# Kernel optimization log

Hardware: AMD Instinct MI355X
Metric: run time of the kernel (lower is better)

The kernel has to match this reference:

```python
import jax, jax.numpy as jnp
import numpy as np

T, H, I, E, K = 2048, 2048, 1408, 8, 2


def setup_inputs() -> dict:
    key = jax.random.key(0)
    k1, k2, k3, k4, k5 = jax.random.split(key, 5)
    s_h = 1.0 / np.sqrt(H)
    s_i = 1.0 / np.sqrt(I)
    return {
        "hidden_states": jax.random.normal(k1, (T, H), dtype=jnp.float32),
        "router_logits": jax.random.normal(k2, (T, E), dtype=jnp.float32),
        "Wg": jax.random.normal(k3, (E, H, I), dtype=jnp.float32) * s_h,
        "Wu": jax.random.normal(k4, (E, H, I), dtype=jnp.float32) * s_h,
        "Wd": jax.random.normal(k5, (E, I, H), dtype=jnp.float32) * s_i,
        "top_k": K,
    }


def reference(hidden_states, router_logits, Wg, Wu, Wd, top_k):
    # top-k routing: softmax over the selected top-k logits (as in torch.topk + softmax)
    topk_vals, topk_ids = jax.lax.top_k(router_logits, top_k)  # [T,K]
    topk_w = jax.nn.softmax(topk_vals, axis=-1)                # [T,K]

    n_tok = hidden_states.shape[0]
    n_exp = router_logits.shape[-1]
    # combine weights [T,E]: scatter top-k weights back to expert slots
    cw = jnp.zeros((n_tok, n_exp), hidden_states.dtype)
    cw = cw.at[jnp.arange(n_tok)[:, None], topk_ids].add(topk_w)

    out = jnp.zeros_like(hidden_states)
    for e in range(n_exp):  # small fixed expert count
        g = hidden_states @ Wg[e]          # [T,I]
        u = hidden_states @ Wu[e]          # [T,I]
        y = (jax.nn.silu(g) * u) @ Wd[e]   # [T,H]
        out = out + cw[:, e:e + 1] * y
    return out
```

## Files before the change

### kernel.cpp

```cpp
#include <hip/hip_runtime.h>
#include <hip/hip_bf16.h>
#include <cstdint>
#include <cstddef>

#define TT 2048
#define HH 2048
#define II 1408
#define EE 8
#define MAXROWS 5120

typedef unsigned short u16;
typedef __attribute__((ext_vector_type(8))) __bf16 bf16x8;
typedef __attribute__((ext_vector_type(4))) float f32x4;

typedef const __attribute__((address_space(1))) uint32_t* gas1_t;
typedef __attribute__((address_space(3))) uint32_t* las3_t;

__device__ __forceinline__ float bf2f(u16 b) {
    return __uint_as_float(((uint32_t)b) << 16);
}
__device__ __forceinline__ u16 f2bf(float x) {
    uint32_t u = __float_as_uint(x);
    u += 0x7fffu + ((u >> 16) & 1u);
    return (u16)(u >> 16);
}

__global__ void k_sniff(const u16* __restrict__ raw, int* __restrict__ flag) {
    __shared__ int cnt;
    if (threadIdx.x == 0) cnt = 0;
    __syncthreads();
    int w = 0;
    for (int i = threadIdx.x; i < 4096; i += 256) {
        u16 x = raw[i];
        if (x & 0x7fff) {
            int ex = (x >> 7) & 0xff;
            if (ex == 0xff || ex < 100 || ex > 140) ++w;
        }
    }
    atomicAdd(&cnt, w);
    __syncthreads();
    if (threadIdx.x == 0) flag[0] = (cnt > 100) ? 1 : 0;
}

__global__ void k_zero(float* __restrict__ out_acc, int* __restrict__ counts) {
    const int i0 = (blockIdx.x * 256 + threadIdx.x) * 4;
    *(float4*)&out_acc[i0] = make_float4(0.f, 0.f, 0.f, 0.f);
    if (blockIdx.x == 0 && threadIdx.x < EE) counts[threadIdx.x] = 0;
}

__global__ void k_routing2(const void* __restrict__ logits, const int* __restrict__ flag,
                           int* __restrict__ counts, int* __restrict__ idx,
                           float* __restrict__ wt) {
    int t = blockIdx.x * 256 + threadIdx.x;
    if (t >= TT) return;
    const int f = flag[0];
    float v[EE];
#pragma unroll
    for (int e = 0; e < EE; ++e)
        v[e] = f ? ((const float*)logits)[t * EE + e]
                 : bf2f(((const u16*)logits)[t * EE + e]);
    int i0 = 0; float v0 = v[0];
#pragma unroll
    for (int e = 1; e < EE; ++e) { if (v[e] > v0) { v0 = v[e]; i0 = e; } }
    int i1 = -1; float v1 = -3.4e38f;
#pragma unroll
    for (int e = 0; e < EE; ++e) { if (e != i0 && v[e] > v1) { v1 = v[e]; i1 = e; } }
    float r = __expf(v1 - v0);
    float s = 1.f / (1.f + r);
    int p0 = atomicAdd(&counts[i0], 1);
    idx[i0 * TT + p0] = t; wt[i0 * TT + p0] = s;
    int p1 = atomicAdd(&counts[i1], 1);
    idx[i1 * TT + p1] = t; wt[i1 * TT + p1] = r * s;
}

__global__ void k_offsets(const int* __restrict__ counts, int* __restrict__ meta) {
    if (threadIdx.x == 0 && blockIdx.x == 0) {
        int off = 0;
        for (int e = 0; e < EE; ++e) {
            int c = counts[e];
            int p = (c + 127) & ~127;
            meta[e] = off; meta[8 + e] = p;
            off += p;
        }
    }
}

__global__ void k_cast(const void* __restrict__ src, const int* __restrict__ flag,
                       u16* __restrict__ dst) {
    const int i0 = (blockIdx.x * 256 + threadIdx.x) * 8;
    if (flag[0]) {
        const float* s = (const float*)src;
#pragma unroll
        for (int j = 0; j < 8; ++j) dst[i0 + j] = f2bf(s[i0 + j]);
    } else {
        const u16* s = (const u16*)src;
        *(uint4*)&dst[i0] = *(const uint4*)&s[i0];
    }
}

__global__ void k_transposeV(const void* __restrict__ src, const int* __restrict__ flag,
                             u16* __restrict__ dst, int R, int C) {
    __shared__ u16 t[64][68];
    const size_t eo = (size_t)blockIdx.z * (size_t)R * (size_t)C;
    const int r0 = blockIdx.y * 64, c0 = blockIdx.x * 64;
    const int tid = threadIdx.x;
    const int f = flag[0];
    {
        const int cg = tid & 15, rr = tid >> 4;
#pragma unroll
        for (int p = 0; p < 4; ++p) {
            const int r = rr + p * 16;
            const size_t base = eo + (size_t)(r0 + r) * C + c0 + cg * 4;
            if (f) {
                const float4 v = *(const float4*)((const float*)src + base);
                t[r][cg * 4 + 0] = f2bf(v.x); t[r][cg * 4 + 1] = f2bf(v.y);
                t[r][cg * 4 + 2] = f2bf(v.z); t[r][cg * 4 + 3] = f2bf(v.w);
            } else {
                const ushort4 v = *(const ushort4*)((const u16*)src + base);
                t[r][cg * 4 + 0] = v.x; t[r][cg * 4 + 1] = v.y;
                t[r][cg * 4 + 2] = v.z; t[r][cg * 4 + 3] = v.w;
            }
        }
    }
    __syncthreads();
    {
        const int rg = tid & 15, cc = tid >> 4;
#pragma unroll
        for (int p = 0; p < 4; ++p) {
            const int c = cc + p * 16;
            ushort4 o;
            o.x = t[rg * 4 + 0][c]; o.y = t[rg * 4 + 1][c];
            o.z = t[rg * 4 + 2][c]; o.w = t[rg * 4 + 3][c];
            *(ushort4*)(dst + eo + (size_t)(c0 + c) * R + r0 + rg * 4) = o;
        }
    }
}

__device__ __forceinline__ void stage16(const u16* __restrict__ g, int stride_elems,
                                        u16* lds, int wave, int lane) {
    const int sub = lane >> 2;
    const int col = (lane & 3) * 8;
#pragma unroll
    for (int h = 0; h < 2; ++h) {
        const int rbase = wave * 32 + h * 16;
        const u16* ga = g + (size_t)(rbase + sub) * stride_elems + col;
        __builtin_amdgcn_global_load_lds((gas1_t)ga, (las3_t)(lds + rbase * 32), 16, 0, 0);
    }
}

__global__ __launch_bounds__(512, 4)
void k_gemm1s(const u16* __restrict__ hs_b,
              const u16* __restrict__ Wgt,
              const u16* __restrict__ Wut,
              const int* __restrict__ counts,
              const int* __restrict__ meta,
              const int* __restrict__ idx,
              const float* __restrict__ wt,
              u16* __restrict__ act_g) {
    const int e = blockIdx.x;
    const int cnt = counts[e];
    const int pcnt = meta[8 + e];
    const int m0 = blockIdx.z * 128;
    if (m0 >= pcnt) return;
    const int n0 = blockIdx.y * 128;
    const int off = meta[e];
    const int tid = threadIdx.x;
    const int wave = tid >> 6, lane = tid & 63;
    const int ln = lane & 15, q = lane >> 4;
    const int wr = (wave >> 2) * 64;
    const int wc = (wave & 3) * 32;

    __shared__ __align__(16) u16 As[128 * 32];
    __shared__ __align__(16) u16 Bg[128 * 32];
    __shared__ __align__(16) u16 Bu[128 * 32];
    __shared__ int   tokS[128];
    __shared__ float wtS[128];

    if (tid < 128) {
        const int pos = m0 + tid;
        const bool v = pos < cnt;
        tokS[tid] = v ? idx[e * TT + pos] : 0;
        wtS[tid]  = v ? wt[e * TT + pos] : 0.f;
    }
    __syncthreads();

    const int srow = tid >> 2;
    const int scol = (tid & 3) * 8;
    const u16* pA = hs_b + (size_t)tokS[srow] * HH + scol;
    const u16* pG = Wgt + ((size_t)e * II + n0 + srow) * HH + scol;
    const u16* pU = Wut + ((size_t)e * II + n0 + srow) * HH + scol;
    u16* const lA = As + srow * 32 + scol;
    u16* const lG = Bg + srow * 32 + scol;
    u16* const lU = Bu + srow * 32 + scol;

    f32x4 accg[4][2], accu[4][2];
#pragma unroll
    for (int mi = 0; mi < 4; ++mi)
#pragma unroll
        for (int ni = 0; ni < 2; ++ni) { accg[mi][ni] = (f32x4)0.f; accu[mi][ni] = (f32x4)0.f; }

    for (int kb = 0; kb < HH; kb += 32) {
        __syncthreads();
        __builtin_amdgcn_global_load_lds((gas1_t)(pA + kb), (las3_t)lA, 16, 0, 0);
        __builtin_amdgcn_global_load_lds((gas1_t)(pG + kb), (las3_t)lG, 16, 0, 0);
        __builtin_amdgcn_global_load_lds((gas1_t)(pU + kb), (las3_t)lU, 16, 0, 0);
        __syncthreads();

        bf16x8 af[4];
#pragma unroll
        for (int mi = 0; mi < 4; ++mi)
            af[mi] = *(const bf16x8*)&As[(wr + mi * 16 + ln) * 32 + q * 8];
#pragma unroll
        for (int ni = 0; ni < 2; ++ni) {
            bf16x8 bgf = *(const bf16x8*)&Bg[(wc + ni * 16 + ln) * 32 + q * 8];
            bf16x8 buf = *(const bf16x8*)&Bu[(wc + ni * 16 + ln) * 32 + q * 8];
#pragma unroll
            for (int mi = 0; mi < 4; ++mi) {
                accg[mi][ni] = __builtin_amdgcn_mfma_f32_16x16x32_bf16(af[mi], bgf, accg[mi][ni], 0, 0, 0);
                accu[mi][ni] = __builtin_amdgcn_mfma_f32_16x16x32_bf16(af[mi], buf, accu[mi][ni], 0, 0, 0);
            }
        }
    }

#pragma unroll
    for (int mi = 0; mi < 4; ++mi) {
#pragma unroll
        for (int r = 0; r < 4; ++r) {
            const int row = wr + mi * 16 + q * 4 + r;
            const float w = wtS[row];
#pragma unroll
            for (int ni = 0; ni < 2; ++ni) {
                const int i = n0 + wc + ni * 16 + ln;
                const float g = accg[mi][ni][r];
                const float u = accu[mi][ni][r];
                const float y = w * u * g / (1.f + __expf(-g));
                act_g[(size_t)(off + m0 + row) * II + i] = f2bf(y);
            }
        }
    }
}

__global__ __launch_bounds__(256, 2)
void k_gemm2s(const u16* __restrict__ act_g,
              const u16* __restrict__ Wdt,
              const int* __restrict__ counts,
              const int* __restrict__ meta,
              const int* __restrict__ idx,
              float* __restrict__ out_acc) {
    const int e = blockIdx.x;
    const int cnt = counts[e];
    const int pcnt = meta[8 + e];
    const int m0 = blockIdx.z * 128;
    if (m0 >= pcnt) return;
    const int n0 = blockIdx.y * 128;
    const int off = meta[e];
    const int tid = threadIdx.x;
    const int wave = tid >> 6, lane = tid & 63;
    const int ln = lane & 15, q = lane >> 4;
    const int wr = (wave >> 1) * 64, wc = (wave & 1) * 64;

    __shared__ __align__(16) u16 As[128 * 32];
    __shared__ __align__(16) u16 Bs[128 * 32];
    __shared__ int tokS[128];

    if (tid < 128) {
        const int pos = m0 + tid;
        tokS[tid] = (pos < cnt) ? idx[e * TT + pos] : -1;
    }

    const u16* bA = act_g + (size_t)(off + m0) * II;
    const u16* bB = Wdt + ((size_t)e * HH + n0) * II;

    f32x4 acc[4][4];
#pragma unroll
    for (int mi = 0; mi < 4; ++mi)
#pragma unroll
        for (int ni = 0; ni < 4; ++ni) acc[mi][ni] = (f32x4)0.f;

    for (int i0 = 0; i0 < II; i0 += 32) {
        __syncthreads();
        stage16(bA + i0, II, As, wave, lane);
        stage16(bB + i0, II, Bs, wave, lane);
        __syncthreads();

        bf16x8 af[4];
#pragma unroll
        for (int mi = 0; mi < 4; ++mi)
            af[mi] = *(const bf16x8*)&As[(wr + mi * 16 + ln) * 32 + q * 8];
#pragma unroll
        for (int ni = 0; ni < 4; ++ni) {
            bf16x8 bf = *(const bf16x8*)&Bs[(wc + ni * 16 + ln) * 32 + q * 8];
#pragma unroll
            for (int mi = 0; mi < 4; ++mi)
                acc[mi][ni] = __builtin_amdgcn_mfma_f32_16x16x32_bf16(af[mi], bf, acc[mi][ni], 0, 0, 0);
        }
    }

#pragma unroll
    for (int mi = 0; mi < 4; ++mi) {
#pragma unroll
        for (int r = 0; r < 4; ++r) {
            const int row = wr + mi * 16 + q * 4 + r;
            const int t = tokS[row];
            if (t >= 0) {
#pragma unroll
                for (int ni = 0; ni < 4; ++ni) {
                    const int h = n0 + wc + ni * 16 + ln;
                    unsafeAtomicAdd(&out_acc[(size_t)t * HH + h], acc[mi][ni][r]);
                }
            }
        }
    }
}

__global__ void k_out(const float* __restrict__ out_acc, const int* __restrict__ flag,
                      void* __restrict__ out) {
    const int i0 = (blockIdx.x * 256 + threadIdx.x) * 4;
    const float4 v = *(const float4*)&out_acc[i0];
    if (flag[0]) {
        *(float4*)((float*)out + i0) = v;
    } else {
        u16* o = (u16*)out + i0;
        o[0] = f2bf(v.x); o[1] = f2bf(v.y); o[2] = f2bf(v.z); o[3] = f2bf(v.w);
    }
}

extern "C" void kernel_launch(void* const* d_in, const int* in_sizes, int n_in,
                              void* d_out, int out_size, void* d_ws, size_t ws_size,
                              hipStream_t stream) {
    (void)in_sizes; (void)n_in; (void)out_size;
    const void* hs     = d_in[0];
    const void* logits = d_in[1];
    const void* Wg     = d_in[2];
    const void* Wu     = d_in[3];
    const void* Wd     = d_in[4];

    char* ws = (char*)d_ws;
    size_t off = 0;
    int*   flag   = (int*)(ws + off);   off += 256;
    int*   counts = (int*)(ws + off);   off += 256;
    int*   meta   = (int*)(ws + off);   off += 256;
    int*   idx    = (int*)(ws + off);   off += (size_t)EE * TT * 4;
    float* wt     = (float*)(ws + off); off += (size_t)EE * TT * 4;
    u16*   hs_b   = (u16*)(ws + off);   off += (size_t)TT * HH * 2;
    u16*   Wgt    = (u16*)(ws + off);   off += (size_t)EE * II * HH * 2;
    u16*   Wut    = (u16*)(ws + off);   off += (size_t)EE * II * HH * 2;
    u16*   Wdt    = (u16*)(ws + off);   off += (size_t)EE * HH * II * 2;
    u16*   act_g  = (u16*)(ws + off);   off += (size_t)MAXROWS * II * 2;
    float* outacc = (float*)(ws + off); off += (size_t)TT * HH * 4;
    if (ws_size < off) return;

    k_sniff<<<dim3(1), dim3(256), 0, stream>>>((const u16*)hs, flag);
    k_zero<<<dim3(TT * HH / (256 * 4)), dim3(256), 0, stream>>>(outacc, counts);
    k_routing2<<<dim3(TT / 256), dim3(256), 0, stream>>>(logits, flag, counts, idx, wt);
    k_offsets<<<dim3(1), dim3(64), 0, stream>>>(counts, meta);
    k_cast<<<dim3(TT * HH / (256 * 8)), dim3(256), 0, stream>>>(hs, flag, hs_b);
    k_transposeV<<<dim3(II / 64, HH / 64, EE), dim3(256), 0, stream>>>(Wg, flag, Wgt, HH, II);
    k_transposeV<<<dim3(II / 64, HH / 64, EE), dim3(256), 0, stream>>>(Wu, flag, Wut, HH, II);
    k_transposeV<<<dim3(HH / 64, II / 64, EE), dim3(256), 0, stream>>>(Wd, flag, Wdt, II, HH);
    k_gemm1s<<<dim3(EE, II / 128, TT / 128), dim3(512), 0, stream>>>(hs_b, Wgt, Wut, counts, meta, idx, wt, act_g);
    k_gemm2s<<<dim3(EE, HH / 128, TT / 128), dim3(256), 0, stream>>>(act_g, Wdt, counts, meta, idx, outacc);
    k_out<<<dim3(TT * HH / (256 * 4)), dim3(256), 0, stream>>>(outacc, flag, d_out);
}
```

Before: 477.2 us.

## Double-buffer GEMM LDS staging, swizzle LDS, replace atomic scatter with gather-combine

Both grouped GEMMs now use two LDS buffers so the next K-slice's global-to-LDS loads are issued before the current slice's MFMAs, with one barrier per iteration instead of two. LDS columns are XOR-swizzled to cut bank conflicts, and expert indices are rotated by block position to spread work across CUs. The down-projection no longer atomically adds into a zeroed fp32 accumulator. It writes per-slot rows to a y buffer, and a combine kernel gathers each token's two slots using a new slot map, which removes the zeroing kernel and the atomics. The cost is a larger fp32 intermediate buffer and doubled LDS use, which may lower occupancy.

```diff
diff --git a/kernel.cpp b/kernel.cpp
--- a/kernel.cpp
+++ b/kernel.cpp
@@ -25,8 +25,10 @@
     return (u16)(u >> 16);
 }
 
-__global__ void k_sniff(const u16* __restrict__ raw, int* __restrict__ flag) {
+__global__ void k_sniff(const u16* __restrict__ raw, int* __restrict__ flag,
+                        int* __restrict__ counts) {
     __shared__ int cnt;
+    if (threadIdx.x < EE) counts[threadIdx.x] = 0;
     if (threadIdx.x == 0) cnt = 0;
     __syncthreads();
     int w = 0;
@@ -42,15 +44,9 @@
     if (threadIdx.x == 0) flag[0] = (cnt > 100) ? 1 : 0;
 }
 
-__global__ void k_zero(float* __restrict__ out_acc, int* __restrict__ counts) {
-    const int i0 = (blockIdx.x * 256 + threadIdx.x) * 4;
-    *(float4*)&out_acc[i0] = make_float4(0.f, 0.f, 0.f, 0.f);
-    if (blockIdx.x == 0 && threadIdx.x < EE) counts[threadIdx.x] = 0;
-}
-
 __global__ void k_routing2(const void* __restrict__ logits, const int* __restrict__ flag,
                            int* __restrict__ counts, int* __restrict__ idx,
-                           float* __restrict__ wt) {
+                           float* __restrict__ wt, int* __restrict__ slot) {
     int t = blockIdx.x * 256 + threadIdx.x;
     if (t >= TT) return;
     const int f = flag[0];
@@ -69,8 +65,10 @@
     float s = 1.f / (1.f + r);
     int p0 = atomicAdd(&counts[i0], 1);
     idx[i0 * TT + p0] = t; wt[i0 * TT + p0] = s;
+    slot[t * 2 + 0] = i0 * TT + p0;
     int p1 = atomicAdd(&counts[i1], 1);
     idx[i1 * TT + p1] = t; wt[i1 * TT + p1] = r * s;
+    slot[t * 2 + 1] = i1 * TT + p1;
 }
 
 __global__ void k_offsets(const int* __restrict__ counts, int* __restrict__ meta) {
@@ -136,17 +134,29 @@
     }
 }
 
-__device__ __forceinline__ void stage16(const u16* __restrict__ g, int stride_elems,
-                                        u16* lds, int wave, int lane) {
-    const int sub = lane >> 2;
-    const int col = (lane & 3) * 8;
-#pragma unroll
-    for (int h = 0; h < 2; ++h) {
-        const int rbase = wave * 32 + h * 16;
-        const u16* ga = g + (size_t)(rbase + sub) * stride_elems + col;
-        __builtin_amdgcn_global_load_lds((gas1_t)ga, (las3_t)(lds + rbase * 32), 16, 0, 0);
-    }
-}
+
+#define G1_COMPUTE(B) do { \
+    bf16x8 af[4]; \
+    _Pragma("unroll") \
+    for (int mi = 0; mi < 4; ++mi) \
+        af[mi] = *(const bf16x8*)&As[B][(wr + mi * 16 + ln) * 32 + qx]; \
+    _Pragma("unroll") \
+    for (int ni = 0; ni < 2; ++ni) { \
+        bf16x8 bgf = *(const bf16x8*)&Bg[B][(wc + ni * 16 + ln) * 32 + qx]; \
+        bf16x8 buf_ = *(const bf16x8*)&Bu[B][(wc + ni * 16 + ln) * 32 + qx]; \
+        _Pragma("unroll") \
+        for (int mi = 0; mi < 4; ++mi) { \
+            accg[mi][ni] = __builtin_amdgcn_mfma_f32_16x16x32_bf16(af[mi], bgf, accg[mi][ni], 0, 0, 0); \
+            accu[mi][ni] = __builtin_amdgcn_mfma_f32_16x16x32_bf16(af[mi], buf_, accu[mi][ni], 0, 0, 0); \
+        } \
+    } \
+} while (0)
+
+#define G1_STAGE(B, KB) do { \
+    __builtin_amdgcn_global_load_lds((gas1_t)(pA + (KB)), (las3_t)(&As[B][dofs]), 16, 0, 0); \
+    __builtin_amdgcn_global_load_lds((gas1_t)(pG + (KB)), (las3_t)(&Bg[B][dofs]), 16, 0, 0); \
+    __builtin_amdgcn_global_load_lds((gas1_t)(pU + (KB)), (las3_t)(&Bu[B][dofs]), 16, 0, 0); \
+} while (0)
 
 __global__ __launch_bounds__(512, 4)
 void k_gemm1s(const u16* __restrict__ hs_b,
@@ -157,7 +167,7 @@
               const int* __restrict__ idx,
               const float* __restrict__ wt,
               u16* __restrict__ act_g) {
-    const int e = blockIdx.x;
+    const int e = (blockIdx.x + blockIdx.y) & 7;
     const int cnt = counts[e];
     const int pcnt = meta[8 + e];
     const int m0 = blockIdx.z * 128;
@@ -170,9 +180,9 @@
     const int wr = (wave >> 2) * 64;
     const int wc = (wave & 3) * 32;
 
-    __shared__ __align__(16) u16 As[128 * 32];
-    __shared__ __align__(16) u16 Bg[128 * 32];
-    __shared__ __align__(16) u16 Bu[128 * 32];
+    __shared__ __align__(16) u16 As[2][128 * 32];
+    __shared__ __align__(16) u16 Bg[2][128 * 32];
+    __shared__ __align__(16) u16 Bu[2][128 * 32];
     __shared__ int   tokS[128];
     __shared__ float wtS[128];
 
@@ -185,13 +195,13 @@
     __syncthreads();
 
     const int srow = tid >> 2;
-    const int scol = (tid & 3) * 8;
-    const u16* pA = hs_b + (size_t)tokS[srow] * HH + scol;
-    const u16* pG = Wgt + ((size_t)e * II + n0 + srow) * HH + scol;
-    const u16* pU = Wut + ((size_t)e * II + n0 + srow) * HH + scol;
-    u16* const lA = As + srow * 32 + scol;
-    u16* const lG = Bg + srow * 32 + scol;
-    u16* const lU = Bu + srow * 32 + scol;
+    const int csw  = (((tid & 3) ^ ((srow >> 1) & 3))) * 8;
+    const u16* pA = hs_b + (size_t)tokS[srow] * HH + csw;
+    const u16* pG = Wgt + ((size_t)e * II + n0 + srow) * HH + csw;
+    const u16* pU = Wut + ((size_t)e * II + n0 + srow) * HH + csw;
+    const int dofs = tid * 8;
+
+    const int qx = (q ^ ((ln >> 1) & 3)) * 8;
 
     f32x4 accg[4][2], accu[4][2];
 #pragma unroll
@@ -199,28 +209,16 @@
 #pragma unroll
         for (int ni = 0; ni < 2; ++ni) { accg[mi][ni] = (f32x4)0.f; accu[mi][ni] = (f32x4)0.f; }
 
-    for (int kb = 0; kb < HH; kb += 32) {
+    G1_STAGE(0, 0);
+    __syncthreads();
+    int cur = 0;
+    for (int kb = 32; kb < HH; kb += 32) {
+        G1_STAGE(cur ^ 1, kb);
+        G1_COMPUTE(cur);
         __syncthreads();
-        __builtin_amdgcn_global_load_lds((gas1_t)(pA + kb), (las3_t)lA, 16, 0, 0);
-        __builtin_amdgcn_global_load_lds((gas1_t)(pG + kb), (las3_t)lG, 16, 0, 0);
-        __builtin_amdgcn_global_load_lds((gas1_t)(pU + kb), (las3_t)lU, 16, 0, 0);
-        __syncthreads();
-
-        bf16x8 af[4];
-#pragma unroll
-        for (int mi = 0; mi < 4; ++mi)
-            af[mi] = *(const bf16x8*)&As[(wr + mi * 16 + ln) * 32 + q * 8];
-#pragma unroll
-        for (int ni = 0; ni < 2; ++ni) {
-            bf16x8 bgf = *(const bf16x8*)&Bg[(wc + ni * 16 + ln) * 32 + q * 8];
-            bf16x8 buf = *(const bf16x8*)&Bu[(wc + ni * 16 + ln) * 32 + q * 8];
-#pragma unroll
-            for (int mi = 0; mi < 4; ++mi) {
-                accg[mi][ni] = __builtin_amdgcn_mfma_f32_16x16x32_bf16(af[mi], bgf, accg[mi][ni], 0, 0, 0);
-                accu[mi][ni] = __builtin_amdgcn_mfma_f32_16x16x32_bf16(af[mi], buf, accu[mi][ni], 0, 0, 0);
-            }
-        }
-    }
+        cur ^= 1;
+    }
+    G1_COMPUTE(cur);
 
 #pragma unroll
     for (int mi = 0; mi < 4; ++mi) {
@@ -240,15 +238,33 @@
     }
 }
 
+#define G2_COMPUTE(B) do { \
+    bf16x8 af[4]; \
+    _Pragma("unroll") \
+    for (int mi = 0; mi < 4; ++mi) \
+        af[mi] = *(const bf16x8*)&As[B][(wr + mi * 16 + ln) * 32 + qx]; \
+    _Pragma("unroll") \
+    for (int ni = 0; ni < 4; ++ni) { \
+        bf16x8 bf = *(const bf16x8*)&Bs[B][(wc + ni * 16 + ln) * 32 + qx]; \
+        _Pragma("unroll") \
+        for (int mi = 0; mi < 4; ++mi) \
+            acc[mi][ni] = __builtin_amdgcn_mfma_f32_16x16x32_bf16(af[mi], bf, acc[mi][ni], 0, 0, 0); \
+    } \
+} while (0)
+
+#define G2_STAGE(B, KB) do { \
+    __builtin_amdgcn_global_load_lds((gas1_t)(pA0 + (KB)), (las3_t)(&As[B][dofs]), 16, 0, 0); \
+    __builtin_amdgcn_global_load_lds((gas1_t)(pA1 + (KB)), (las3_t)(&As[B][2048 + dofs]), 16, 0, 0); \
+    __builtin_amdgcn_global_load_lds((gas1_t)(pB0 + (KB)), (las3_t)(&Bs[B][dofs]), 16, 0, 0); \
+    __builtin_amdgcn_global_load_lds((gas1_t)(pB1 + (KB)), (las3_t)(&Bs[B][2048 + dofs]), 16, 0, 0); \
+} while (0)
+
 __global__ __launch_bounds__(256, 2)
 void k_gemm2s(const u16* __restrict__ act_g,
               const u16* __restrict__ Wdt,
-              const int* __restrict__ counts,
               const int* __restrict__ meta,
-              const int* __restrict__ idx,
-              float* __restrict__ out_acc) {
-    const int e = blockIdx.x;
-    const int cnt = counts[e];
+              float* __restrict__ y_g) {
+    const int e = (blockIdx.x + blockIdx.y) & 7;
     const int pcnt = meta[8 + e];
     const int m0 = blockIdx.z * 128;
     if (m0 >= pcnt) return;
@@ -259,17 +275,20 @@
     const int ln = lane & 15, q = lane >> 4;
     const int wr = (wave >> 1) * 64, wc = (wave & 1) * 64;
 
-    __shared__ __align__(16) u16 As[128 * 32];
-    __shared__ __align__(16) u16 Bs[128 * 32];
-    __shared__ int tokS[128];
-
-    if (tid < 128) {
-        const int pos = m0 + tid;
-        tokS[tid] = (pos < cnt) ? idx[e * TT + pos] : -1;
-    }
-
+    __shared__ __align__(16) u16 As[2][128 * 32];
+    __shared__ __align__(16) u16 Bs[2][128 * 32];
+
+    const int srow = tid >> 2;
+    const int csw  = (((tid & 3) ^ ((srow >> 1) & 3))) * 8;
     const u16* bA = act_g + (size_t)(off + m0) * II;
     const u16* bB = Wdt + ((size_t)e * HH + n0) * II;
+    const u16* pA0 = bA + (size_t)srow * II + csw;
+    const u16* pA1 = bA + (size_t)(srow + 64) * II + csw;
+    const u16* pB0 = bB + (size_t)srow * II + csw;
+    const u16* pB1 = bB + (size_t)(srow + 64) * II + csw;
+    const int dofs = tid * 8;
+
+    const int qx = (q ^ ((ln >> 1) & 3)) * 8;
 
     f32x4 acc[4][4];
 #pragma unroll
@@ -277,50 +296,46 @@
 #pragma unroll
         for (int ni = 0; ni < 4; ++ni) acc[mi][ni] = (f32x4)0.f;
 
-    for (int i0 = 0; i0 < II; i0 += 32) {
+    G2_STAGE(0, 0);
+    __syncthreads();
+    int cur = 0;
+    for (int kb = 32; kb < II; kb += 32) {
+        G2_STAGE(cur ^ 1, kb);
+        G2_COMPUTE(cur);
         __syncthreads();
-        stage16(bA + i0, II, As, wave, lane);
-        stage16(bB + i0, II, Bs, wave, lane);
-        __syncthreads();
-
-        bf16x8 af[4];
-#pragma unroll
-        for (int mi = 0; mi < 4; ++mi)
-            af[mi] = *(const bf16x8*)&As[(wr + mi * 16 + ln) * 32 + q * 8];
-#pragma unroll
-        for (int ni = 0; ni < 4; ++ni) {
-            bf16x8 bf = *(const bf16x8*)&Bs[(wc + ni * 16 + ln) * 32 + q * 8];
-#pragma unroll
-            for (int mi = 0; mi < 4; ++mi)
-                acc[mi][ni] = __builtin_amdgcn_mfma_f32_16x16x32_bf16(af[mi], bf, acc[mi][ni], 0, 0, 0);
-        }
-    }
+        cur ^= 1;
+    }
+    G2_COMPUTE(cur);
 
 #pragma unroll
     for (int mi = 0; mi < 4; ++mi) {
 #pragma unroll
         for (int r = 0; r < 4; ++r) {
             const int row = wr + mi * 16 + q * 4 + r;
-            const int t = tokS[row];
-            if (t >= 0) {
-#pragma unroll
-                for (int ni = 0; ni < 4; ++ni) {
-                    const int h = n0 + wc + ni * 16 + ln;
-                    unsafeAtomicAdd(&out_acc[(size_t)t * HH + h], acc[mi][ni][r]);
-                }
-            }
-        }
-    }
-}
-
-__global__ void k_out(const float* __restrict__ out_acc, const int* __restrict__ flag,
-                      void* __restrict__ out) {
-    const int i0 = (blockIdx.x * 256 + threadIdx.x) * 4;
-    const float4 v = *(const float4*)&out_acc[i0];
+            float* dst = y_g + (size_t)(off + m0 + row) * HH + n0 + wc;
+#pragma unroll
+            for (int ni = 0; ni < 4; ++ni)
+                dst[ni * 16 + ln] = acc[mi][ni][r];
+        }
+    }
+}
+
+__global__ void k_combine(const float* __restrict__ y_g, const int* __restrict__ slot,
+                          const int* __restrict__ meta, const int* __restrict__ flag,
+                          void* __restrict__ out) {
+    const int gid = blockIdx.x * 256 + threadIdx.x;
+    const int t = gid >> 9;
+    const int h = (gid & 511) * 4;
+    const int s0 = slot[t * 2 + 0], s1 = slot[t * 2 + 1];
+    const int r0 = meta[s0 >> 11] + (s0 & 2047);
+    const int r1 = meta[s1 >> 11] + (s1 & 2047);
+    const float4 a = *(const float4*)&y_g[(size_t)r0 * HH + h];
+    const float4 b = *(const float4*)&y_g[(size_t)r1 * HH + h];
+    const float4 v = make_float4(a.x + b.x, a.y + b.y, a.z + b.z, a.w + b.w);
     if (flag[0]) {
-        *(float4*)((float*)out + i0) = v;
+        *(float4*)((float*)out + (size_t)t * HH + h) = v;
     } else {
-        u16* o = (u16*)out + i0;
+        u16* o = (u16*)out + (size_t)t * HH + h;
         o[0] = f2bf(v.x); o[1] = f2bf(v.y); o[2] = f2bf(v.z); o[3] = f2bf(v.w);
     }
 }
@@ -342,23 +357,23 @@
     int*   meta   = (int*)(ws + off);   off += 256;
     int*   idx    = (int*)(ws + off);   off += (size_t)EE * TT * 4;
     float* wt     = (float*)(ws + off); off += (size_t)EE * TT * 4;
+    int*   slot   = (int*)(ws + off);   off += (size_t)TT * 2 * 4;
     u16*   hs_b   = (u16*)(ws + off);   off += (size_t)TT * HH * 2;
     u16*   Wgt    = (u16*)(ws + off);   off += (size_t)EE * II * HH * 2;
     u16*   Wut    = (u16*)(ws + off);   off += (size_t)EE * II * HH * 2;
     u16*   Wdt    = (u16*)(ws + off);   off += (size_t)EE * HH * II * 2;
     u16*   act_g  = (u16*)(ws + off);   off += (size_t)MAXROWS * II * 2;
-    float* outacc = (float*)(ws + off); off += (size_t)TT * HH * 4;
+    float* y_g    = (float*)(ws + off); off += (size_t)MAXROWS * HH * 4;
     if (ws_size < off) return;
 
-    k_sniff<<<dim3(1), dim3(256), 0, stream>>>((const u16*)hs, flag);
-    k_zero<<<dim3(TT * HH / (256 * 4)), dim3(256), 0, stream>>>(outacc, counts);
-    k_routing2<<<dim3(TT / 256), dim3(256), 0, stream>>>(logits, flag, counts, idx, wt);
+    k_sniff<<<dim3(1), dim3(256), 0, stream>>>((const u16*)hs, flag, counts);
+    k_routing2<<<dim3(TT / 256), dim3(256), 0, stream>>>(logits, flag, counts, idx, wt, slot);
     k_offsets<<<dim3(1), dim3(64), 0, stream>>>(counts, meta);
     k_cast<<<dim3(TT * HH / (256 * 8)), dim3(256), 0, stream>>>(hs, flag, hs_b);
     k_transposeV<<<dim3(II / 64, HH / 64, EE), dim3(256), 0, stream>>>(Wg, flag, Wgt, HH, II);
     k_transposeV<<<dim3(II / 64, HH / 64, EE), dim3(256), 0, stream>>>(Wu, flag, Wut, HH, II);
     k_transposeV<<<dim3(HH / 64, II / 64, EE), dim3(256), 0, stream>>>(Wd, flag, Wdt, II, HH);
     k_gemm1s<<<dim3(EE, II / 128, TT / 128), dim3(512), 0, stream>>>(hs_b, Wgt, Wut, counts, meta, idx, wt, act_g);
-    k_gemm2s<<<dim3(EE, HH / 128, TT / 128), dim3(256), 0, stream>>>(act_g, Wdt, counts, meta, idx, outacc);
-    k_out<<<dim3(TT * HH / (256 * 4)), dim3(256), 0, stream>>>(outacc, flag, d_out);
-}
+    k_gemm2s<<<dim3(EE, HH / 128, TT / 128), dim3(256), 0, stream>>>(act_g, Wdt, meta, y_g);
+    k_combine<<<dim3(TT * HH / (256 * 4)), dim3(256), 0, stream>>>(y_g, slot, meta, flag, d_out);
+}
```

Result: faster. 464.6 us (-2.6%).
